# Kernel optimization log

Measured on AMD Instinct MI355X. Metric: run time of the kernel, lower is better.

## Reference

```python
import jax, jax.numpy as jnp
import numpy as np

NX, NY = 8192, 8192
C1, C2, D = 2048, 2048, 512

def setup_inputs() -> dict:
    key = jax.random.key(0)
    k1, k2, k3, k4, k5 = jax.random.split(key, 5)
    scale1 = 1.0 / np.sqrt(C1)
    scale2 = 1.0 / np.sqrt(C2)
    return {
        "x": jax.random.normal(k1, (NX, C1), dtype=jnp.float32),
        "y": jax.random.normal(k2, (NY, C2), dtype=jnp.float32),
        "Wq": jax.random.uniform(k3, (D, C1), dtype=jnp.float32, minval=-scale1, maxval=scale1),
        "Wk": jax.random.uniform(k4, (D, C2), dtype=jnp.float32, minval=-scale2, maxval=scale2),
        "Wv": jax.random.uniform(k5, (D, C2), dtype=jnp.float32, minval=-scale2, maxval=scale2),
    }

def reference(x, y, Wq, Wk, Wv):
    d = Wq.shape[0]
    q = x @ Wq.T                      # [nx, d]
    k = y @ Wk.T                      # [ny, d]
    v = y @ Wv.T                      # [ny, d]
    a = (q @ k.T) * (d ** -0.5)       # [nx, ny]
    # torch.triu(ones) masks upper triangle INCLUDING diagonal -> zero where j >= i
    nx, ny = a.shape
    i = jnp.arange(nx)[:, None]
    j = jnp.arange(ny)[None, :]
    a = jnp.where(j >= i, 0.0, a)
    return a @ v                      # [nx, d]
```

## Files before the change

kernel.cpp:

```cpp
#include <hip/hip_runtime.h>
#include <hip/hip_bf16.h>


typedef __bf16 bf16x8 __attribute__((ext_vector_type(8)));
typedef __bf16 bf16x4 __attribute__((ext_vector_type(4)));
typedef float f32x4 __attribute__((ext_vector_type(4)));

#define MFMA16(a, b, c) __builtin_amdgcn_mfma_f32_16x16x32_bf16(a, b, c, 0, 0, 0)

constexpr float SCALE = 0.04419417382415922f;

__device__ __forceinline__ void ld16(const void* g, void* l) {
    __builtin_amdgcn_global_load_lds(
        (__attribute__((address_space(1))) void*)g,
        (__attribute__((address_space(3))) void*)l, 16, 0, 0);
}

__device__ __forceinline__ bf16x8 frag(const __bf16* base, int r, int c) {
    return *(const bf16x8*)((const char*)base + r * 128 + ((c ^ (r & 7)) * 16));
}

__device__ __forceinline__ bf16x8 fragA32(const float* base, int r, int fq) {
    const char* rowp = (const char*)base + r * 128;
    const int c0 = fq * 2;
    f32x4 a = *(const f32x4*)(rowp + ((c0 ^ (r & 7)) * 16));
    f32x4 b = *(const f32x4*)(rowp + (((c0 + 1) ^ (r & 7)) * 16));
    bf16x8 o;
    o[0] = (__bf16)a[0]; o[1] = (__bf16)a[1];
    o[2] = (__bf16)a[2]; o[3] = (__bf16)a[3];
    o[4] = (__bf16)b[0]; o[5] = (__bf16)b[1];
    o[6] = (__bf16)b[2]; o[7] = (__bf16)b[3];
    return o;
}

__device__ __forceinline__ bf16x8 fragB32(const __bf16* base, int r, int fq) {
    return *(const bf16x8*)((const char*)base + r * 64 + ((fq ^ (r & 3)) * 16));
}

__device__ inline bf16x4 pack4(float4 a) {
    bf16x4 r;
    r[0] = (__bf16)a.x; r[1] = (__bf16)a.y;
    r[2] = (__bf16)a.z; r[3] = (__bf16)a.w;
    return r;
}

__global__ __launch_bounds__(256) void convert_w(
    const float* __restrict__ wqf, const float* __restrict__ wkf,
    const float* __restrict__ wvf, __bf16* __restrict__ wqb,
    __bf16* __restrict__ wkb, __bf16* __restrict__ wvb)
{
    const size_t tid = (size_t)blockIdx.x * 256 + threadIdx.x;
    const size_t w = tid >> 6;
    const int lane = (int)(tid & 63);
    size_t f = w * 512;
    const float* src; __bf16* dst;
    if (f < 1048576)      { src = wqf; dst = wqb; }
    else if (f < 2097152) { src = wkf; dst = wkb; f -= 1048576; }
    else                  { src = wvf; dst = wvb; f -= 2097152; }
    const float4* s4 = (const float4*)(src + f);
    float4 a = s4[lane];
    float4 b = s4[64 + lane];
    __bf16* d = dst + f;
    *(bf16x4*)(d + lane * 4)       = pack4(a);
    *(bf16x4*)(d + 256 + lane * 4) = pack4(b);
}

__global__ __launch_bounds__(256, 2) void gemm_qkv2(
    const float* __restrict__ x, const float* __restrict__ y,
    const __bf16* __restrict__ wq, const __bf16* __restrict__ wk,
    const __bf16* __restrict__ wv, __bf16* __restrict__ qo,
    __bf16* __restrict__ ko, __bf16* __restrict__ kT,
    __bf16* __restrict__ vT)
{
    constexpr int K = 2048, N = 512;
    __shared__ __align__(16) float  Asf[2][128][32];
    __shared__ __align__(16) __bf16 Bs[2][2][128][32];

    const bool iskv = (blockIdx.y & 1) != 0;
    const float* A = iskv ? y : x;
    const __bf16* B0 = iskv ? wk : wq;

    const int tid  = threadIdx.x;
    const int wave = tid >> 6, lane = tid & 63;
    const int fr = lane & 15, fq = lane >> 4;
    const int m0 = blockIdx.x * 128, n0 = (blockIdx.y >> 1) * 128;
    const int wr = (wave >> 1) * 64, wc = (wave & 1) * 64;
    const int lr  = lane >> 3;
    const int cd  = (lane & 7) ^ lr;
    const int lr2 = lane >> 2;
    const int cb  = (lane & 3) ^ (lr2 & 3);

    f32x4 acc0[4][4], acc1[4][4];
#pragma unroll
    for (int a = 0; a < 4; ++a)
#pragma unroll
        for (int b = 0; b < 4; ++b) {
            acc0[a][b] = f32x4{0.f, 0.f, 0.f, 0.f};
            acc1[a][b] = f32x4{0.f, 0.f, 0.f, 0.f};
        }

    const float*  ag  = A  + (size_t)(m0 + wave * 32 + lr) * K + cd * 4;
    const __bf16* bg0 = B0 + (size_t)(n0 + wave * 32 + lr2) * K + cb * 8;
    const __bf16* bg1 = wv + (size_t)(n0 + wave * 32 + lr2) * K + cb * 8;

    auto stg = [&](int kks, int buf) {
        float* al = &Asf[buf][wave * 32][0];
#pragma unroll
        for (int u = 0; u < 4; ++u)
            ld16(ag + (size_t)(u * 8) * K + kks, al + u * 256);
        __bf16* b0 = &Bs[buf][0][wave * 32][0];
#pragma unroll
        for (int u = 0; u < 2; ++u)
            ld16(bg0 + (size_t)(u * 16) * K + kks, b0 + u * 512);
        if (iskv) {
            __bf16* b1 = &Bs[buf][1][wave * 32][0];
#pragma unroll
            for (int u = 0; u < 2; ++u)
                ld16(bg1 + (size_t)(u * 16) * K + kks, b1 + u * 512);
        }
    };

    stg(0, 0);
    __syncthreads();

    for (int s = 0; s < 64; ++s) {
        const int buf = s & 1;
        if (s < 63) stg((s + 1) * 32, buf ^ 1);

        bf16x8 af[4], bf[4];
#pragma unroll
        for (int rt = 0; rt < 4; ++rt)
            af[rt] = fragA32(&Asf[buf][0][0], wr + rt * 16 + fr, fq);
#pragma unroll
        for (int nt = 0; nt < 4; ++nt)
            bf[nt] = fragB32(&Bs[buf][0][0][0], wc + nt * 16 + fr, fq);
#pragma unroll
        for (int rt = 0; rt < 4; ++rt)
#pragma unroll
            for (int nt = 0; nt < 4; ++nt)
                acc0[rt][nt] = MFMA16(af[rt], bf[nt], acc0[rt][nt]);
        if (iskv) {
            bf16x8 bv[4];
#pragma unroll
            for (int nt = 0; nt < 4; ++nt)
                bv[nt] = fragB32(&Bs[buf][1][0][0], wc + nt * 16 + fr, fq);
#pragma unroll
            for (int rt = 0; rt < 4; ++rt)
#pragma unroll
                for (int nt = 0; nt < 4; ++nt)
                    acc1[rt][nt] = MFMA16(af[rt], bv[nt], acc1[rt][nt]);
        }
        __syncthreads();
    }

    if (!iskv) {
#pragma unroll
        for (int rt = 0; rt < 4; ++rt)
#pragma unroll
            for (int nt = 0; nt < 4; ++nt) {
                const int col = n0 + wc + nt * 16 + fr;
#pragma unroll
                for (int r = 0; r < 4; ++r) {
                    const int row = m0 + wr + rt * 16 + fq * 4 + r;
                    qo[(size_t)row * N + col] = (__bf16)(acc0[rt][nt][r] * SCALE);
                }
            }
    } else {
#pragma unroll
        for (int rt = 0; rt < 4; ++rt)
#pragma unroll
            for (int nt = 0; nt < 4; ++nt) {
                const int col  = n0 + wc + nt * 16 + fr;
                const int row0 = m0 + wr + rt * 16 + fq * 4;
                bf16x4 k4, v4;
#pragma unroll
                for (int r = 0; r < 4; ++r) {
                    k4[r] = (__bf16)acc0[rt][nt][r];
                    v4[r] = (__bf16)acc1[rt][nt][r];
                    ko[(size_t)(row0 + r) * N + col] = k4[r];
                }
                *(bf16x4*)(kT + (size_t)col * 8192 + row0) = k4;
                *(bf16x4*)(vT + (size_t)col * 8192 + row0) = v4;
            }
    }
}

__global__ __launch_bounds__(256, 3) void hs_gemm(
    const __bf16* __restrict__ vT, const __bf16* __restrict__ kT,
    const __bf16* __restrict__ q, const __bf16* __restrict__ k,
    __bf16* __restrict__ Ht, __bf16* __restrict__ Sd)
{
    __shared__ __align__(16) __bf16 As[128][64];
    __shared__ __align__(16) __bf16 Bs[128][64];

    const int tid  = threadIdx.x;
    const int wave = tid >> 6, lane = tid & 63;
    const int fr = lane & 15, fq = lane >> 4;
    const int wr = (wave >> 1) * 64, wc = (wave & 1) * 64;
    const int lr = lane >> 3;
    const int cd = (lane & 7) ^ lr;

    f32x4 acc[4][4];
#pragma unroll
    for (int a = 0; a < 4; ++a)
#pragma unroll
        for (int b = 0; b < 4; ++b) acc[a][b] = f32x4{0.f, 0.f, 0.f, 0.f};

    __bf16* al = &As[wave * 32][0];
    __bf16* bl = &Bs[wave * 32][0];

    if (blockIdx.y < 63) {
        const int c  = blockIdx.y;
        const int m0 = (blockIdx.x & 3) * 128;
        const int n0 = (blockIdx.x >> 2) * 128;

        const __bf16* ag = vT + (size_t)(m0 + wave * 32 + lr) * 8192 + c * 128 + cd * 8;
        const __bf16* bg = kT + (size_t)(n0 + wave * 32 + lr) * 8192 + c * 128 + cd * 8;

        for (int kk = 0; kk < 128; kk += 64) {
            __syncthreads();
#pragma unroll
            for (int u = 0; u < 4; ++u) {
                ld16(ag + (size_t)(u * 8) * 8192 + kk, al + u * 512);
                ld16(bg + (size_t)(u * 8) * 8192 + kk, bl + u * 512);
            }
            __syncthreads();
#pragma unroll
            for (int ks = 0; ks < 2; ++ks) {
                bf16x8 af[4], bf[4];
#pragma unroll
                for (int rt = 0; rt < 4; ++rt)
                    af[rt] = frag(&As[0][0], wr + rt * 16 + fr, ks * 4 + fq);
#pragma unroll
                for (int nt = 0; nt < 4; ++nt)
                    bf[nt] = frag(&Bs[0][0], wc + nt * 16 + fr, ks * 4 + fq);
#pragma unroll
                for (int rt = 0; rt < 4; ++rt)
#pragma unroll
                    for (int nt = 0; nt < 4; ++nt)
                        acc[rt][nt] = MFMA16(af[rt], bf[nt], acc[rt][nt]);
            }
        }

        __bf16* tp = Ht + (size_t)c * 262144;
#pragma unroll
        for (int rt = 0; rt < 4; ++rt)
#pragma unroll
            for (int nt = 0; nt < 4; ++nt) {
                const int col = n0 + wc + nt * 16 + fr;
#pragma unroll
                for (int r = 0; r < 4; ++r) {
                    const int row = m0 + wr + rt * 16 + fq * 4 + r;
                    tp[(size_t)row * 512 + col] = (__bf16)acc[rt][nt][r];
                }
            }
    } else {
        const int t = (blockIdx.y - 63) * 16 + blockIdx.x;

        const __bf16* ag = q + (size_t)(t * 128 + wave * 32 + lr) * 512 + cd * 8;
        const __bf16* bg = k + (size_t)(t * 128 + wave * 32 + lr) * 512 + cd * 8;

        for (int kk = 0; kk < 512; kk += 64) {
            __syncthreads();
#pragma unroll
            for (int u = 0; u < 4; ++u) {
                ld16(ag + (size_t)(u * 8) * 512 + kk, al + u * 512);
                ld16(bg + (size_t)(u * 8) * 512 + kk, bl + u * 512);
            }
            __syncthreads();
#pragma unroll
            for (int ks = 0; ks < 2; ++ks) {
                bf16x8 af[4], bf[4];
#pragma unroll
                for (int rt = 0; rt < 4; ++rt)
                    af[rt] = frag(&As[0][0], wr + rt * 16 + fr, ks * 4 + fq);
#pragma unroll
                for (int nt = 0; nt < 4; ++nt)
                    bf[nt] = frag(&Bs[0][0], wc + nt * 16 + fr, ks * 4 + fq);
#pragma unroll
                for (int rt = 0; rt < 4; ++rt)
#pragma unroll
                    for (int nt = 0; nt < 4; ++nt)
                        acc[rt][nt] = MFMA16(af[rt], bf[nt], acc[rt][nt]);
            }
        }

        __bf16* tp = Sd + (size_t)t * 16384;
#pragma unroll
        for (int rt = 0; rt < 4; ++rt)
#pragma unroll
            for (int nt = 0; nt < 4; ++nt) {
                const int col = wc + nt * 16 + fr;
#pragma unroll
                for (int r = 0; r < 4; ++r) {
                    const int row = wr + rt * 16 + fq * 4 + r;
                    float vv = (col < row) ? acc[rt][nt][r] : 0.f;
                    tp[row * 128 + col] = (__bf16)vv;
                }
            }
    }
}

__global__ __launch_bounds__(256) void prefix_scan(
    const __bf16* __restrict__ Ht, __bf16* __restrict__ Pt)
{
    const size_t e = ((size_t)blockIdx.x * 256 + threadIdx.x) * 4;
    float a0 = 0.f, a1 = 0.f, a2 = 0.f, a3 = 0.f;
#pragma unroll 7
    for (int c = 0; c < 63; ++c) {
        bf16x4 h = *(const bf16x4*)(Ht + (size_t)c * 262144 + e);
        a0 += (float)h[0]; a1 += (float)h[1];
        a2 += (float)h[2]; a3 += (float)h[3];
        bf16x4 p;
        p[0] = (__bf16)a0; p[1] = (__bf16)a1;
        p[2] = (__bf16)a2; p[3] = (__bf16)a3;
        *(bf16x4*)(Pt + (size_t)(c + 1) * 262144 + e) = p;
    }
}

__global__ __launch_bounds__(256, 2) void out_gemm(
    const __bf16* __restrict__ q, const __bf16* __restrict__ Sd,
    const __bf16* __restrict__ vT, const __bf16* __restrict__ Pt,
    float* __restrict__ out)
{
    __shared__ __align__(16) __bf16 As[2][128][64];
    __shared__ __align__(16) __bf16 Bs[2][128][64];

    const int t  = blockIdx.x;
    const int n0 = blockIdx.y * 128;

    const int tid  = threadIdx.x;
    const int wave = tid >> 6, lane = tid & 63;
    const int fr = lane & 15, fq = lane >> 4;
    const int wr = (wave >> 1) * 64, wc = (wave & 1) * 64;
    const int lr = lane >> 3;
    const int cd = (lane & 7) ^ lr;
    const int srow = wave * 32 + lr;

    f32x4 acc[4][4];
#pragma unroll
    for (int a = 0; a < 4; ++a)
#pragma unroll
        for (int b = 0; b < 4; ++b) acc[a][b] = f32x4{0.f, 0.f, 0.f, 0.f};

    const __bf16* qB  = q  + (size_t)(t * 128 + srow) * 512 + cd * 8;
    const __bf16* ptB = Pt + (size_t)t * 262144 + (size_t)(n0 + srow) * 512 + cd * 8;
    const __bf16* sdB = Sd + (size_t)t * 16384 + (size_t)srow * 128 + cd * 8;
    const __bf16* vtB = vT + (size_t)(n0 + srow) * 8192 + t * 128 + cd * 8;

    const int ns = (t > 0) ? 10 : 2;

    auto stg = [&](int s, int buf) {
        const __bf16 *ap, *bp; size_t sa, sb;
        if (t > 0 && s < 8) { ap = qB + s * 64;  sa = 512;  bp = ptB + s * 64; sb = 512; }
        else { const int sc = (t > 0) ? s - 8 : s;
               ap = sdB + sc * 64; sa = 128; bp = vtB + sc * 64; sb = 8192; }
        __bf16* al = &As[buf][wave * 32][0];
        __bf16* bl = &Bs[buf][wave * 32][0];
#pragma unroll
        for (int u = 0; u < 4; ++u) {
            ld16(ap + (size_t)(u * 8) * sa, al + u * 512);
            ld16(bp + (size_t)(u * 8) * sb, bl + u * 512);
        }
    };

    stg(0, 0);
    __syncthreads();

    for (int s = 0; s < ns; ++s) {
        const int buf = s & 1;
        if (s + 1 < ns) stg(s + 1, buf ^ 1);
#pragma unroll
        for (int ks = 0; ks < 2; ++ks) {
            bf16x8 af[4], bf[4];
#pragma unroll
            for (int rt = 0; rt < 4; ++rt)
                af[rt] = frag(&As[buf][0][0], wr + rt * 16 + fr, ks * 4 + fq);
#pragma unroll
            for (int nt = 0; nt < 4; ++nt)
                bf[nt] = frag(&Bs[buf][0][0], wc + nt * 16 + fr, ks * 4 + fq);
#pragma unroll
            for (int rt = 0; rt < 4; ++rt)
#pragma unroll
                for (int nt = 0; nt < 4; ++nt)
                    acc[rt][nt] = MFMA16(af[rt], bf[nt], acc[rt][nt]);
        }
        __syncthreads();
    }

#pragma unroll
    for (int rt = 0; rt < 4; ++rt)
#pragma unroll
        for (int nt = 0; nt < 4; ++nt) {
            const int col = n0 + wc + nt * 16 + fr;
#pragma unroll
            for (int r = 0; r < 4; ++r) {
                const int row = t * 128 + wr + rt * 16 + fq * 4 + r;
                out[(size_t)row * 512 + col] = acc[rt][nt][r];
            }
        }
}

extern "C" void kernel_launch(void* const* d_in, const int* in_sizes, int n_in,
                              void* d_out, int out_size, void* d_ws, size_t ws_size,
                              hipStream_t stream) {
    const float* x  = (const float*)d_in[0];
    const float* y  = (const float*)d_in[1];
    const float* Wq = (const float*)d_in[2];
    const float* Wk = (const float*)d_in[3];
    const float* Wv = (const float*)d_in[4];
    float* out = (float*)d_out;

    const size_t QK = (size_t)8192 * 512;
    __bf16* q  = (__bf16*)d_ws;
    __bf16* k  = q + QK;
    __bf16* kT = k + QK;
    __bf16* vT = kT + QK;
    __bf16* Ht  = vT + QK;
    __bf16* Pt  = Ht + 16777216;
    __bf16* wqb = Pt + 16777216;
    __bf16* wkb = wqb + 1048576;
    __bf16* wvb = wkb + 1048576;
    __bf16* Sd = wqb;

    convert_w<<<1536, 256, 0, stream>>>(Wq, Wk, Wv, wqb, wkb, wvb);
    gemm_qkv2<<<dim3(64, 8), 256, 0, stream>>>(x, y, wqb, wkb, wvb, q, k, kT, vT);
    hs_gemm<<<dim3(16, 67), 256, 0, stream>>>(vT, kT, q, k, Ht, Sd);
    prefix_scan<<<256, 256, 0, stream>>>(Ht, Pt);
    out_gemm<<<dim3(64, 4), 256, 0, stream>>>(q, Sd, vT, Pt, out);
}
```

Baseline: 275.4 us.

## Give Q-projection blocks a 128x256 output tile to balance work with KV blocks

The QKV projection grid changes from 8 to 6 y-blocks. Each Q block now computes two adjacent 128-column output tiles against the same staged x tile, so Q and KV blocks do equal MFMA work and Q re-reads x half as often. The B staging is unified into one 128x64 bf16 LDS tile per buffer, filled with per-lane global-to-LDS loads and read with the existing swizzled frag helper. The cost is that every block now always holds two accumulator sets, which raises register pressure, and the grid has fewer blocks.

```diff
diff --git a/kernel.cpp b/kernel.cpp
--- a/kernel.cpp
+++ b/kernel.cpp
@@ -20,21 +20,16 @@
     return *(const bf16x8*)((const char*)base + r * 128 + ((c ^ (r & 7)) * 16));
 }
 
-__device__ __forceinline__ bf16x8 fragA32(const float* base, int r, int fq) {
+__device__ __forceinline__ bf16x8 fragA(const float* base, int r, int fq) {
     const char* rowp = (const char*)base + r * 128;
-    const int c0 = fq * 2;
-    f32x4 a = *(const f32x4*)(rowp + ((c0 ^ (r & 7)) * 16));
-    f32x4 b = *(const f32x4*)(rowp + (((c0 + 1) ^ (r & 7)) * 16));
+    f32x4 a = *(const f32x4*)(rowp + (((2 * fq)     ^ (r & 7)) * 16));
+    f32x4 b = *(const f32x4*)(rowp + (((2 * fq + 1) ^ (r & 7)) * 16));
     bf16x8 o;
     o[0] = (__bf16)a[0]; o[1] = (__bf16)a[1];
     o[2] = (__bf16)a[2]; o[3] = (__bf16)a[3];
     o[4] = (__bf16)b[0]; o[5] = (__bf16)b[1];
     o[6] = (__bf16)b[2]; o[7] = (__bf16)b[3];
     return o;
-}
-
-__device__ __forceinline__ bf16x8 fragB32(const __bf16* base, int r, int fq) {
-    return *(const bf16x8*)((const char*)base + r * 64 + ((fq ^ (r & 3)) * 16));
 }
 
 __device__ inline bf16x4 pack4(float4 a) {
@@ -74,21 +69,30 @@
 {
     constexpr int K = 2048, N = 512;
     __shared__ __align__(16) float  Asf[2][128][32];
-    __shared__ __align__(16) __bf16 Bs[2][2][128][32];
-
-    const bool iskv = (blockIdx.y & 1) != 0;
+    __shared__ __align__(16) __bf16 Bs[2][128][64];
+
+    const int gy = blockIdx.y;
+    const bool iskv = gy >= 2;
     const float* A = iskv ? y : x;
-    const __bf16* B0 = iskv ? wk : wq;
+    int n0a, n0b;
+    const __bf16 *B0, *B1;
+    if (iskv) {
+        n0a = (gy - 2) * 128; n0b = n0a;
+        B0 = wk + (size_t)n0a * K;
+        B1 = wv + (size_t)n0a * K;
+    } else {
+        n0a = gy * 256; n0b = n0a + 128;
+        B0 = wq + (size_t)n0a * K;
+        B1 = wq + (size_t)n0b * K;
+    }
 
     const int tid  = threadIdx.x;
     const int wave = tid >> 6, lane = tid & 63;
     const int fr = lane & 15, fq = lane >> 4;
-    const int m0 = blockIdx.x * 128, n0 = (blockIdx.y >> 1) * 128;
+    const int m0 = blockIdx.x * 128;
     const int wr = (wave >> 1) * 64, wc = (wave & 1) * 64;
-    const int lr  = lane >> 3;
-    const int cd  = (lane & 7) ^ lr;
-    const int lr2 = lane >> 2;
-    const int cb  = (lane & 3) ^ (lr2 & 3);
+    const int lr = lane >> 3;
+    const int cc = (lane & 7) ^ lr;
 
     f32x4 acc0[4][4], acc1[4][4];
 #pragma unroll
@@ -99,24 +103,21 @@
             acc1[a][b] = f32x4{0.f, 0.f, 0.f, 0.f};
         }
 
-    const float*  ag  = A  + (size_t)(m0 + wave * 32 + lr) * K + cd * 4;
-    const __bf16* bg0 = B0 + (size_t)(n0 + wave * 32 + lr2) * K + cb * 8;
-    const __bf16* bg1 = wv + (size_t)(n0 + wave * 32 + lr2) * K + cb * 8;
+    const float*  aSrc[4];
+    const __bf16* bSrc[4];
+#pragma unroll
+    for (int u = 0; u < 4; ++u) {
+        const int rw = wave * 32 + u * 8 + lr;
+        aSrc[u] = A + (size_t)(m0 + rw) * K + cc * 4;
+        const __bf16* bsel = (cc < 4) ? B0 : B1;
+        bSrc[u] = bsel + (size_t)rw * K + (cc & 3) * 8;
+    }
 
     auto stg = [&](int kks, int buf) {
-        float* al = &Asf[buf][wave * 32][0];
-#pragma unroll
-        for (int u = 0; u < 4; ++u)
-            ld16(ag + (size_t)(u * 8) * K + kks, al + u * 256);
-        __bf16* b0 = &Bs[buf][0][wave * 32][0];
-#pragma unroll
-        for (int u = 0; u < 2; ++u)
-            ld16(bg0 + (size_t)(u * 16) * K + kks, b0 + u * 512);
-        if (iskv) {
-            __bf16* b1 = &Bs[buf][1][wave * 32][0];
-#pragma unroll
-            for (int u = 0; u < 2; ++u)
-                ld16(bg1 + (size_t)(u * 16) * K + kks, b1 + u * 512);
+#pragma unroll
+        for (int u = 0; u < 4; ++u) {
+            ld16(aSrc[u] + kks, &Asf[buf][wave * 32 + u * 8][0] + lane * 4);
+            ld16(bSrc[u] + kks, &Bs[buf][wave * 32 + u * 8][0] + lane * 8);
         }
     };
 
@@ -127,29 +128,22 @@
         const int buf = s & 1;
         if (s < 63) stg((s + 1) * 32, buf ^ 1);
 
-        bf16x8 af[4], bf[4];
-#pragma unroll
-        for (int rt = 0; rt < 4; ++rt)
-            af[rt] = fragA32(&Asf[buf][0][0], wr + rt * 16 + fr, fq);
-#pragma unroll
-        for (int nt = 0; nt < 4; ++nt)
-            bf[nt] = fragB32(&Bs[buf][0][0][0], wc + nt * 16 + fr, fq);
-#pragma unroll
-        for (int rt = 0; rt < 4; ++rt)
-#pragma unroll
-            for (int nt = 0; nt < 4; ++nt)
-                acc0[rt][nt] = MFMA16(af[rt], bf[nt], acc0[rt][nt]);
-        if (iskv) {
-            bf16x8 bv[4];
-#pragma unroll
-            for (int nt = 0; nt < 4; ++nt)
-                bv[nt] = fragB32(&Bs[buf][1][0][0], wc + nt * 16 + fr, fq);
-#pragma unroll
-            for (int rt = 0; rt < 4; ++rt)
-#pragma unroll
-                for (int nt = 0; nt < 4; ++nt)
-                    acc1[rt][nt] = MFMA16(af[rt], bv[nt], acc1[rt][nt]);
-        }
+        bf16x8 af[4], b0[4], b1[4];
+#pragma unroll
+        for (int rt = 0; rt < 4; ++rt)
+            af[rt] = fragA(&Asf[buf][0][0], wr + rt * 16 + fr, fq);
+#pragma unroll
+        for (int nt = 0; nt < 4; ++nt) {
+            b0[nt] = frag(&Bs[buf][0][0], wc + nt * 16 + fr, fq);
+            b1[nt] = frag(&Bs[buf][0][0], wc + nt * 16 + fr, 4 + fq);
+        }
+#pragma unroll
+        for (int rt = 0; rt < 4; ++rt)
+#pragma unroll
+            for (int nt = 0; nt < 4; ++nt) {
+                acc0[rt][nt] = MFMA16(af[rt], b0[nt], acc0[rt][nt]);
+                acc1[rt][nt] = MFMA16(af[rt], b1[nt], acc1[rt][nt]);
+            }
         __syncthreads();
     }
 
@@ -158,11 +152,13 @@
         for (int rt = 0; rt < 4; ++rt)
 #pragma unroll
             for (int nt = 0; nt < 4; ++nt) {
-                const int col = n0 + wc + nt * 16 + fr;
+                const int ca = n0a + wc + nt * 16 + fr;
+                const int cb = n0b + wc + nt * 16 + fr;
 #pragma unroll
                 for (int r = 0; r < 4; ++r) {
                     const int row = m0 + wr + rt * 16 + fq * 4 + r;
-                    qo[(size_t)row * N + col] = (__bf16)(acc0[rt][nt][r] * SCALE);
+                    qo[(size_t)row * N + ca] = (__bf16)(acc0[rt][nt][r] * SCALE);
+                    qo[(size_t)row * N + cb] = (__bf16)(acc1[rt][nt][r] * SCALE);
                 }
             }
     } else {
@@ -170,7 +166,7 @@
         for (int rt = 0; rt < 4; ++rt)
 #pragma unroll
             for (int nt = 0; nt < 4; ++nt) {
-                const int col  = n0 + wc + nt * 16 + fr;
+                const int col  = n0a + wc + nt * 16 + fr;
                 const int row0 = m0 + wr + rt * 16 + fq * 4;
                 bf16x4 k4, v4;
 #pragma unroll
@@ -424,7 +420,7 @@
     __bf16* Sd = wqb;
 
     convert_w<<<1536, 256, 0, stream>>>(Wq, Wk, Wv, wqb, wkb, wvb);
-    gemm_qkv2<<<dim3(64, 8), 256, 0, stream>>>(x, y, wqb, wkb, wvb, q, k, kT, vT);
+    gemm_qkv2<<<dim3(64, 6), 256, 0, stream>>>(x, y, wqb, wkb, wvb, q, k, kT, vT);
     hs_gemm<<<dim3(16, 67), 256, 0, stream>>>(vT, kT, q, k, Ht, Sd);
     prefix_scan<<<256, 256, 0, stream>>>(Ht, Pt);
     out_gemm<<<dim3(64, 4), 256, 0, stream>>>(q, Sd, vT, Pt, out);
```

Measured after the change: 295.4 us. 1.07x slower.
